# Kernel optimization log

Hardware: AMD Instinct MI355X
Metric: run time of the kernel (lower is better)

The kernel has to match this reference:

```python
import jax, jax.numpy as jnp
import numpy as np

N, M, D_IN, D_TXT, D_OUT, H = 4096, 1024, 512, 512, 512, 8
DH = D_OUT // H


def positional_encoding(n, dim):
    # Matches PositionalEncoding: freq = exp((arange(dim//2)/dim)*ln(10000)),
    # x = pos/freq -> [L, dim//2], interleave (sin, cos) pairs -> [L, dim].
    pos = jnp.arange(n, dtype=jnp.float32)
    freq = jnp.exp((jnp.arange(dim // 2, dtype=jnp.float32) / dim) * jnp.log(jnp.float32(10000.0)))
    x = pos[:, None] / freq  # [L, dim//2]
    pe = jnp.stack((jnp.sin(x), jnp.cos(x)), axis=-1)  # [L, dim//2, 2]
    return pe.reshape(n, dim)


def setup_inputs() -> dict:
    key = jax.random.key(0)
    k1, k2, k3, k4, k5, k6 = jax.random.split(key, 6)
    s = 0.02
    return {
        "video_features": jax.random.normal(k1, (N, D_IN), dtype=jnp.float32),
        "text_features": jax.random.normal(k2, (M, D_TXT), dtype=jnp.float32),
        "Wq": jax.random.normal(k3, (H, D_IN, DH), dtype=jnp.float32) * s,
        "Wk": jax.random.normal(k4, (H, D_TXT, DH), dtype=jnp.float32) * s,
        "Wv": jax.random.normal(k5, (H, D_TXT, DH), dtype=jnp.float32) * s,
        "Wout": jax.random.normal(k6, (D_OUT, D_IN), dtype=jnp.float32) * s,
    }


def reference(video_features, text_features, Wq, Wk, Wv, Wout):
    # Batched over heads instead of the original per-head Python loop (same math).
    Q = jnp.einsum('nd,hde->hne', video_features, Wq)   # [H, N, DH]
    K = jnp.einsum('md,hde->hme', text_features, Wk)    # [H, M, DH]
    V = jnp.einsum('md,hde->hme', text_features, Wv)    # [H, M, DH]
    energies = jnp.einsum('hne,hme->hnm', Q, K)         # no scaling in original
    att = jax.nn.softmax(energies, axis=-1)             # dropout omitted (eval mode)
    y = jnp.einsum('hnm,hme->hne', att, V)              # [H, N, DH]
    y = jnp.transpose(y, (1, 0, 2)).reshape(video_features.shape[0], -1)  # concat heads
    y = y @ Wout                                        # [N, D_IN]
    y = y + positional_encoding(y.shape[0], y.shape[1])
    return y
```

## Files before the change

kernel.cpp:

```cpp
#include <hip/hip_runtime.h>
#include <hip/hip_bf16.h>
#include <math.h>

#define N_TOK 4096
#define M_TOK 1024
#define DMODEL 512
#define NHEAD 8
#define DHEAD 64

typedef __attribute__((ext_vector_type(8))) short short8;
typedef __attribute__((ext_vector_type(4))) float f32x4;
typedef __attribute__((ext_vector_type(4))) float float4v;

static __device__ __forceinline__ short f2bf(float f) {
    union { float f; unsigned u; } v; v.f = f;
    unsigned r = v.u + 0x7fffu + ((v.u >> 16) & 1u);
    return (short)(r >> 16);
}

#define GLOAD_LDS16(g, l) __builtin_amdgcn_global_load_lds( \
    (const __attribute__((address_space(1))) void*)(g), \
    (__attribute__((address_space(3))) void*)(l), 16, 0, 0)

__global__ __launch_bounds__(256) void pack_kernel(
        const float* __restrict__ xv, const float* __restrict__ xt,
        const float* __restrict__ wq, const float* __restrict__ wk,
        const float* __restrict__ wv, const float* __restrict__ wo,
        short* __restrict__ xvb, short* __restrict__ xtb,
        short* __restrict__ wqb, short* __restrict__ wkb,
        short* __restrict__ wvb, short* __restrict__ wob) {
    int bid = blockIdx.x;
    int t = threadIdx.x;
    if (bid < 256) {
        __shared__ float lds[64][65];
        const float* src;
        short* dst;
        int srstride;
        int dr0, dc0;
        if (bid < 192) {
            int mat = bid >> 6;
            int hb = bid & 63;
            int h = hb >> 3, dt = hb & 7;
            const float* W = (mat == 0) ? wq : (mat == 1) ? wk : wv;
            src = W + (size_t)h * (DMODEL * DHEAD) + (size_t)(dt * 64) * DHEAD;
            srstride = DHEAD;
            dst = (mat == 0) ? wqb : (mat == 1) ? wkb : wvb;
            dr0 = h * 64;
            dc0 = dt * 64;
        } else {
            int b = bid - 192;
            int rt = b >> 3, ct = b & 7;
            src = wo + (size_t)(rt * 64) * DMODEL + ct * 64;
            srstride = DMODEL;
            dst = wob;
            dr0 = ct * 64;
            dc0 = rt * 64;
        }
        {
            int r = t >> 2, c0 = (t & 3) * 16;
            const float* s = src + (size_t)r * srstride + c0;
            #pragma unroll
            for (int j = 0; j < 4; j++) {
                float4v v = *(const float4v*)(s + j * 4);
                lds[r][c0 + j * 4 + 0] = v[0];
                lds[r][c0 + j * 4 + 1] = v[1];
                lds[r][c0 + j * 4 + 2] = v[2];
                lds[r][c0 + j * 4 + 3] = v[3];
            }
        }
        __syncthreads();
        {
            int outr = t >> 2, c0 = (t & 3) * 16;
            short8 o0, o1;
            #pragma unroll
            for (int j = 0; j < 8; j++) {
                o0[j] = f2bf(lds[c0 + j][outr]);
                o1[j] = f2bf(lds[c0 + 8 + j][outr]);
            }
            short* d = dst + (size_t)(dr0 + outr) * DMODEL + dc0 + c0;
            *(short8*)d = o0;
            *(short8*)(d + 8) = o1;
        }
        return;
    }
    int idx = (bid - 256) * 256 + t;
    int stride = (gridDim.x - 256) * 256;
    const int CXV = N_TOK * DMODEL / 8;
    const int CXT = M_TOK * DMODEL / 8;
    for (int c = idx; c < CXV; c += stride) {
        float4v f0 = *(const float4v*)&xv[c * 8];
        float4v f1 = *(const float4v*)&xv[c * 8 + 4];
        short8 o;
        #pragma unroll
        for (int j = 0; j < 4; j++) { o[j] = f2bf(f0[j]); o[j + 4] = f2bf(f1[j]); }
        *(short8*)&xvb[c * 8] = o;
    }
    for (int c = idx; c < CXT; c += stride) {
        float4v f0 = *(const float4v*)&xt[c * 8];
        float4v f1 = *(const float4v*)&xt[c * 8 + 4];
        short8 o;
        #pragma unroll
        for (int j = 0; j < 4; j++) { o[j] = f2bf(f0[j]); o[j + 4] = f2bf(f1[j]); }
        *(short8*)&xtb[c * 8] = o;
    }
}

template<typename EPI>
static __device__ __forceinline__ void gemm_body(const short* __restrict__ A,
                                                 const short* __restrict__ BT,
                                                 int m0, int n0, EPI epi) {
    __shared__ __align__(16) short As[64][72];
    __shared__ __align__(16) short Bs[64][72];
    int t = threadIdx.x;
    int lane = t & 63, w = t >> 6;
    int wr = w >> 1, wc = w & 1;
    int l15 = lane & 15, g = lane >> 4;

    int row = t >> 2, c0 = (t & 3) * 16;
    const short* gA = A + (size_t)(m0 + row) * DMODEL + c0;
    const short* gB = BT + (size_t)(n0 + row) * DMODEL + c0;

    short8 ra0 = *(const short8*)gA;
    short8 ra1 = *(const short8*)(gA + 8);
    short8 rb0 = *(const short8*)gB;
    short8 rb1 = *(const short8*)(gB + 8);

    f32x4 acc[2][2] = {};
    #pragma unroll
    for (int step = 0; step < DMODEL / 64; ++step) {
        *(short8*)&As[row][c0]     = ra0;
        *(short8*)&As[row][c0 + 8] = ra1;
        *(short8*)&Bs[row][c0]     = rb0;
        *(short8*)&Bs[row][c0 + 8] = rb1;
        __syncthreads();
        if (step < DMODEL / 64 - 1) {
            gA += 64; gB += 64;
            ra0 = *(const short8*)gA;
            ra1 = *(const short8*)(gA + 8);
            rb0 = *(const short8*)gB;
            rb1 = *(const short8*)(gB + 8);
        }
        #pragma unroll
        for (int ks = 0; ks < 2; ks++) {
            short8 a[2], b[2];
            #pragma unroll
            for (int fr = 0; fr < 2; fr++) a[fr] = *(short8*)&As[wr * 32 + fr * 16 + l15][ks * 32 + g * 8];
            #pragma unroll
            for (int fc = 0; fc < 2; fc++) b[fc] = *(short8*)&Bs[wc * 32 + fc * 16 + l15][ks * 32 + g * 8];
            #pragma unroll
            for (int fr = 0; fr < 2; fr++)
                #pragma unroll
                for (int fc = 0; fc < 2; fc++)
                    acc[fr][fc] = __builtin_amdgcn_mfma_f32_16x16x32_bf16(a[fr], b[fc], acc[fr][fc], 0, 0, 0);
        }
        __syncthreads();
    }
    #pragma unroll
    for (int fr = 0; fr < 2; fr++)
        #pragma unroll
        for (int fc = 0; fc < 2; fc++)
            #pragma unroll
            for (int r = 0; r < 4; r++) {
                int orow = m0 + wr * 32 + fr * 16 + g * 4 + r;
                int ocol = n0 + wc * 32 + fc * 16 + l15;
                epi(orow, ocol, acc[fr][fc][r]);
            }
}

__global__ __launch_bounds__(256) void gemmQKV(const short* __restrict__ xvb,
                                               const short* __restrict__ xtb,
                                               const short* __restrict__ wqb,
                                               const short* __restrict__ wkb,
                                               const short* __restrict__ wvb,
                                               short* __restrict__ qb,
                                               short* __restrict__ kbm,
                                               short* __restrict__ vbt) {
    int bx = blockIdx.x;
    int n0 = blockIdx.y * 64;
    if (bx < 64) {
        short* C = qb;
        gemm_body(xvb, wqb, bx * 64, n0,
                  [&](int row, int col, float v) { C[(size_t)row * DMODEL + col] = f2bf(v); });
    } else if (bx < 80) {
        short* C = kbm;
        gemm_body(xtb, wkb, (bx - 64) * 64, n0,
                  [&](int row, int col, float v) { C[(size_t)row * DMODEL + col] = f2bf(v); });
    } else {
        short* C = vbt;
        gemm_body(xtb, wvb, (bx - 80) * 64, n0,
                  [&](int row, int col, float v) { C[(size_t)col * M_TOK + row] = f2bf(v); });
    }
}

__global__ __launch_bounds__(256) void gemmOut(const short* __restrict__ A,
                                               const short* __restrict__ BT,
                                               float* __restrict__ Cout) {
    __shared__ float ifreq[256];
    ifreq[threadIdx.x] = __expf(-(float)threadIdx.x * (9.210340371976184f / 512.0f));
    __syncthreads();
    gemm_body(A, BT, blockIdx.x * 64, blockIdx.y * 64,
              [&](int row, int col, float v) {
                  float x = (float)row * ifreq[col >> 1];
                  float s, c;
                  __sincosf(x, &s, &c);
                  Cout[(size_t)row * DMODEL + col] = v + ((col & 1) ? c : s);
              });
}

__global__ __launch_bounds__(256) void attn_kernel(const short* __restrict__ Qb,
                                                   const short* __restrict__ Kb,
                                                   const short* __restrict__ VbT,
                                                   short* __restrict__ Yb) {
    __shared__ __align__(16) short Ks[2][64][64];
    __shared__ __align__(16) short Vs[2][64][64];
    __shared__ __align__(16) short Ps[4][16][72];

    int bid = blockIdx.x;
    int h = bid & 7;
    int n0 = (bid >> 3) * 64;
    int t = threadIdx.x;
    int lane = t & 63, w = t >> 6;
    int l15 = lane & 15, g = lane >> 4;

    const short* Kh  = Kb + h * DHEAD;
    const short* VhT = VbT + (h * DHEAD) * M_TOK;

    int srow = (lane >> 3);
    int sgran = (lane & 7) ^ srow;
    const short* gK0 = Kh + (size_t)(w * 16 + srow) * DMODEL + sgran * 8;
    const short* gV0 = VhT + (size_t)(w * 16 + srow) * M_TOK + sgran * 8;

    const short* qrow = Qb + (size_t)(n0 + w * 16 + l15) * DMODEL + h * DHEAD;
    short8 qa0 = *(const short8*)(qrow + g * 8);
    short8 qa1 = *(const short8*)(qrow + 32 + g * 8);

    f32x4 acc[4] = {};
    f32x4 rsum = {};
    int sx = l15 & 7;

    GLOAD_LDS16(gK0,              &Ks[0][w * 16][0]);
    GLOAD_LDS16(gK0 + 8 * DMODEL, &Ks[0][w * 16 + 8][0]);
    GLOAD_LDS16(gV0,              &Vs[0][w * 16][0]);
    GLOAD_LDS16(gV0 + 8 * M_TOK,  &Vs[0][w * 16 + 8][0]);
    __syncthreads();

    int buf = 0;
    for (int it = 0; it < 16; ++it) {
        if (it < 15) {
            int key0 = (it + 1) * 64;
            GLOAD_LDS16(gK0 + (size_t)key0 * DMODEL,       &Ks[buf ^ 1][w * 16][0]);
            GLOAD_LDS16(gK0 + (size_t)(key0 + 8) * DMODEL, &Ks[buf ^ 1][w * 16 + 8][0]);
            GLOAD_LDS16(gV0 + key0,                        &Vs[buf ^ 1][w * 16][0]);
            GLOAD_LDS16(gV0 + key0 + 8 * M_TOK,            &Vs[buf ^ 1][w * 16 + 8][0]);
        }
        #pragma unroll
        for (int kt = 0; kt < 4; kt++) {
            short8 kf0 = *(short8*)&Ks[buf][kt * 16 + l15][((g) ^ sx) * 8];
            short8 kf1 = *(short8*)&Ks[buf][kt * 16 + l15][((4 + g) ^ sx) * 8];
            f32x4 e = {};
            e = __builtin_amdgcn_mfma_f32_16x16x32_bf16(qa0, kf0, e, 0, 0, 0);
            e = __builtin_amdgcn_mfma_f32_16x16x32_bf16(qa1, kf1, e, 0, 0, 0);
            #pragma unroll
            for (int r = 0; r < 4; r++) {
                float p = exp2f(e[r] * 1.44269504f);
                rsum[r] += p;
                Ps[w][g * 4 + r][kt * 16 + l15] = f2bf(p);
            }
        }
        #pragma unroll
        for (int kb2 = 0; kb2 < 2; kb2++) {
            short8 pa = *(short8*)&Ps[w][l15][kb2 * 32 + g * 8];
            #pragma unroll
            for (int nt = 0; nt < 4; nt++) {
                short8 vf = *(short8*)&Vs[buf][nt * 16 + l15][((kb2 * 4 + g) ^ sx) * 8];
                acc[nt] = __builtin_amdgcn_mfma_f32_16x16x32_bf16(pa, vf, acc[nt], 0, 0, 0);
            }
        }
        __syncthreads();
        buf ^= 1;
    }

    #pragma unroll
    for (int r = 0; r < 4; r++) {
        float s = rsum[r];
        s += __shfl_xor(s, 1);
        s += __shfl_xor(s, 2);
        s += __shfl_xor(s, 4);
        s += __shfl_xor(s, 8);
        rsum[r] = s;
    }

    #pragma unroll
    for (int nt = 0; nt < 4; nt++)
        #pragma unroll
        for (int r = 0; r < 4; r++) {
            float y = acc[nt][r] / rsum[r];
            Yb[(size_t)(n0 + w * 16 + g * 4 + r) * DMODEL + h * DHEAD + nt * 16 + l15] = f2bf(y);
        }
}

extern "C" void kernel_launch(void* const* d_in, const int* in_sizes, int n_in,
                              void* d_out, int out_size, void* d_ws, size_t ws_size,
                              hipStream_t stream) {
    const float* xv = (const float*)d_in[0];
    const float* xt = (const float*)d_in[1];
    const float* wq = (const float*)d_in[2];
    const float* wk = (const float*)d_in[3];
    const float* wv = (const float*)d_in[4];
    const float* wo = (const float*)d_in[5];

    short* xvb = (short*)d_ws;
    short* xtb = xvb + N_TOK * DMODEL;
    short* wqb = xtb + M_TOK * DMODEL;
    short* wkb = wqb + DMODEL * DMODEL;
    short* wvb = wkb + DMODEL * DMODEL;
    short* wob = wvb + DMODEL * DMODEL;
    short* qb  = wob + DMODEL * DMODEL;
    short* kbm = qb  + N_TOK * DMODEL;
    short* vbt = kbm + M_TOK * DMODEL;
    short* yb  = vbt + M_TOK * DMODEL;

    pack_kernel<<<1280, 256, 0, stream>>>(xv, xt, wq, wk, wv, wo,
                                          xvb, xtb, wqb, wkb, wvb, wob);
    gemmQKV<<<dim3(96, 8), 256, 0, stream>>>(xvb, xtb, wqb, wkb, wvb, qb, kbm, vbt);
    attn_kernel<<<512, 256, 0, stream>>>(qb, kbm, vbt, yb);
    gemmOut<<<dim3(64, 8), 256, 0, stream>>>(yb, wob, (float*)d_out);
}
```

Baseline: 58.45 us.

## Replace async global-to-LDS double buffer with register-staged single-buffer K/V tiles

The attention kernel drops the global_load_lds double-buffered, XOR-swizzled K/V tiles. It now prefetches the next tile into registers and stores them into a single padded LDS buffer at the top of each iteration, with a barrier. This halves LDS use, which can raise occupancy, and avoids the direct-to-LDS load path. In exchange it adds VGPR pressure, an extra barrier per iteration, and register-to-LDS store traffic.

```diff
diff --git a/kernel.cpp b/kernel.cpp
--- a/kernel.cpp
+++ b/kernel.cpp
@@ -17,10 +17,6 @@
     unsigned r = v.u + 0x7fffu + ((v.u >> 16) & 1u);
     return (short)(r >> 16);
 }
-
-#define GLOAD_LDS16(g, l) __builtin_amdgcn_global_load_lds( \
-    (const __attribute__((address_space(1))) void*)(g), \
-    (__attribute__((address_space(3))) void*)(l), 16, 0, 0)
 
 __global__ __launch_bounds__(256) void pack_kernel(
         const float* __restrict__ xv, const float* __restrict__ xt,
@@ -211,8 +207,8 @@
                                                    const short* __restrict__ Kb,
                                                    const short* __restrict__ VbT,
                                                    short* __restrict__ Yb) {
-    __shared__ __align__(16) short Ks[2][64][64];
-    __shared__ __align__(16) short Vs[2][64][64];
+    __shared__ __align__(16) short Ks[64][72];
+    __shared__ __align__(16) short Vt[64][72];
     __shared__ __align__(16) short Ps[4][16][72];
 
     int bid = blockIdx.x;
@@ -222,13 +218,14 @@
     int lane = t & 63, w = t >> 6;
     int l15 = lane & 15, g = lane >> 4;
 
-    const short* Kh  = Kb + h * DHEAD;
-    const short* VhT = VbT + (h * DHEAD) * M_TOK;
-
-    int srow = (lane >> 3);
-    int sgran = (lane & 7) ^ srow;
-    const short* gK0 = Kh + (size_t)(w * 16 + srow) * DMODEL + sgran * 8;
-    const short* gV0 = VhT + (size_t)(w * 16 + srow) * M_TOK + sgran * 8;
+    int row = t >> 2, c0 = (t & 3) * 16;
+    const short* gK = Kb + (size_t)row * DMODEL + h * DHEAD + c0;
+    const short* gV = VbT + (size_t)(h * DHEAD + row) * M_TOK + c0;
+
+    short8 k0 = *(const short8*)gK;
+    short8 k1 = *(const short8*)(gK + 8);
+    short8 v0 = *(const short8*)gV;
+    short8 v1 = *(const short8*)(gV + 8);
 
     const short* qrow = Qb + (size_t)(n0 + w * 16 + l15) * DMODEL + h * DHEAD;
     short8 qa0 = *(const short8*)(qrow + g * 8);
@@ -236,27 +233,25 @@
 
     f32x4 acc[4] = {};
     f32x4 rsum = {};
-    int sx = l15 & 7;
-
-    GLOAD_LDS16(gK0,              &Ks[0][w * 16][0]);
-    GLOAD_LDS16(gK0 + 8 * DMODEL, &Ks[0][w * 16 + 8][0]);
-    GLOAD_LDS16(gV0,              &Vs[0][w * 16][0]);
-    GLOAD_LDS16(gV0 + 8 * M_TOK,  &Vs[0][w * 16 + 8][0]);
-    __syncthreads();
-
-    int buf = 0;
+
     for (int it = 0; it < 16; ++it) {
+        *(short8*)&Ks[row][c0]     = k0;
+        *(short8*)&Ks[row][c0 + 8] = k1;
+        *(short8*)&Vt[row][c0]     = v0;
+        *(short8*)&Vt[row][c0 + 8] = v1;
+        __syncthreads();
         if (it < 15) {
-            int key0 = (it + 1) * 64;
-            GLOAD_LDS16(gK0 + (size_t)key0 * DMODEL,       &Ks[buf ^ 1][w * 16][0]);
-            GLOAD_LDS16(gK0 + (size_t)(key0 + 8) * DMODEL, &Ks[buf ^ 1][w * 16 + 8][0]);
-            GLOAD_LDS16(gV0 + key0,                        &Vs[buf ^ 1][w * 16][0]);
-            GLOAD_LDS16(gV0 + key0 + 8 * M_TOK,            &Vs[buf ^ 1][w * 16 + 8][0]);
+            gK += (size_t)64 * DMODEL;
+            gV += 64;
+            k0 = *(const short8*)gK;
+            k1 = *(const short8*)(gK + 8);
+            v0 = *(const short8*)gV;
+            v1 = *(const short8*)(gV + 8);
         }
         #pragma unroll
         for (int kt = 0; kt < 4; kt++) {
-            short8 kf0 = *(short8*)&Ks[buf][kt * 16 + l15][((g) ^ sx) * 8];
-            short8 kf1 = *(short8*)&Ks[buf][kt * 16 + l15][((4 + g) ^ sx) * 8];
+            short8 kf0 = *(short8*)&Ks[kt * 16 + l15][g * 8];
+            short8 kf1 = *(short8*)&Ks[kt * 16 + l15][32 + g * 8];
             f32x4 e = {};
             e = __builtin_amdgcn_mfma_f32_16x16x32_bf16(qa0, kf0, e, 0, 0, 0);
             e = __builtin_amdgcn_mfma_f32_16x16x32_bf16(qa1, kf1, e, 0, 0, 0);
@@ -272,12 +267,11 @@
             short8 pa = *(short8*)&Ps[w][l15][kb2 * 32 + g * 8];
             #pragma unroll
             for (int nt = 0; nt < 4; nt++) {
-                short8 vf = *(short8*)&Vs[buf][nt * 16 + l15][((kb2 * 4 + g) ^ sx) * 8];
+                short8 vf = *(short8*)&Vt[nt * 16 + l15][kb2 * 32 + g * 8];
                 acc[nt] = __builtin_amdgcn_mfma_f32_16x16x32_bf16(pa, vf, acc[nt], 0, 0, 0);
             }
         }
         __syncthreads();
-        buf ^= 1;
     }
 
     #pragma unroll
```

After: 58.75 us. No clear change (+0.5%).
